# Kernel optimization log

Hardware: AMD Instinct MI355X
Metric: run time of the kernel (lower is better)

## Reference

```python
import jax, jax.numpy as jnp
import numpy as np

N_NODES = 100000
BN_EPS = 1e-5


def _linear_params(key, fan_in, fan_out):
    k1, k2 = jax.random.split(key)
    lim = 1.0 / np.sqrt(fan_in)
    W = jax.random.uniform(k1, (fan_in, fan_out), jnp.float32, -lim, lim)
    b = jax.random.uniform(k2, (fan_out,), jnp.float32, -lim, lim)
    return W, b


def setup_inputs() -> dict:
    key = jax.random.key(0)
    ks = jax.random.split(key, 24)
    in_ch, hid, tdim, L = 17, 64, 32, 2
    E = 1600000
    inp = {}
    inp["x"] = jax.random.normal(ks[0], (N_NODES, in_ch), jnp.float32)
    inp["edge_index"] = jax.random.randint(ks[1], (2, E), 0, N_NODES, jnp.int64)
    inp["edge_dts"] = jax.random.uniform(ks[2], (E,), jnp.float32) * 100.0
    inp["batch_size"] = 10000
    # TimeEncode params (learned, TGAT init)
    inp["basis_freq"] = jnp.asarray(1.0 / 10 ** np.linspace(0, 9, tdim), jnp.float32)
    inp["phase"] = jnp.zeros((tdim,), jnp.float32)
    # TMP edge MLP: in = 2*in_ch + tdim
    mi = 2 * in_ch + tdim
    inp["tmp_W1"], inp["tmp_b1"] = _linear_params(ks[3], mi, mi // 2)
    inp["tmp_W2"], inp["tmp_b2"] = _linear_params(ks[4], mi // 2, in_ch)
    inp["proj_W"], inp["proj_b"] = _linear_params(ks[5], in_ch, hid)
    # SMP layers (stacked over L)
    si = 2 * hid
    W1s, b1s, W2s, b2s = [], [], [], []
    for l in range(L):
        W1, b1 = _linear_params(ks[6 + 2 * l], si, si // 2)
        W2, b2 = _linear_params(ks[7 + 2 * l], si // 2, hid)
        W1s.append(W1); b1s.append(b1); W2s.append(W2); b2s.append(b2)
    inp["smp_W1"] = jnp.stack(W1s); inp["smp_b1"] = jnp.stack(b1s)
    inp["smp_W2"] = jnp.stack(W2s); inp["smp_b2"] = jnp.stack(b2s)
    inp["bn_gamma"] = jnp.ones((L, hid), jnp.float32)
    inp["bn_beta"] = jnp.zeros((L, hid), jnp.float32)
    # classifier head
    inp["clf_W1"], inp["clf_b1"] = _linear_params(ks[12], hid, hid)
    inp["clf_g1"] = jnp.ones((hid,), jnp.float32); inp["clf_bb1"] = jnp.zeros((hid,), jnp.float32)
    inp["clf_W2"], inp["clf_b2"] = _linear_params(ks[13], hid, hid // 2)
    inp["clf_g2"] = jnp.ones((hid // 2,), jnp.float32); inp["clf_bb2"] = jnp.zeros((hid // 2,), jnp.float32)
    inp["clf_W3"], inp["clf_b3"] = _linear_params(ks[14], hid // 2, 1)
    return inp


def _segment_mean(vals, idx, n):
    s = jax.ops.segment_sum(vals, idx, num_segments=n)
    c = jax.ops.segment_sum(jnp.ones((idx.shape[0], 1), vals.dtype), idx, num_segments=n)
    return s / jnp.maximum(c, 1.0)


def _bn(x, g, b):
    m = x.mean(0)
    v = x.var(0)
    return (x - m) * jax.lax.rsqrt(v + BN_EPS) * g + b


def reference(x, edge_index, edge_dts, batch_size, basis_freq, phase,
              tmp_W1, tmp_b1, tmp_W2, tmp_b2, proj_W, proj_b,
              smp_W1, smp_b1, smp_W2, smp_b2, bn_gamma, bn_beta,
              clf_W1, clf_b1, clf_g1, clf_bb1,
              clf_W2, clf_b2, clf_g2, clf_bb2, clf_W3, clf_b3):
    src, dst = edge_index[0], edge_index[1]  # x_j = x[src], x_i = x[dst]
    n = x.shape[0]
    # TimeEncode: cos(t * freq + phase)  -> [E, time_dim]
    rel = jnp.cos(edge_dts[:, None] * basis_freq + phase)
    # --- TMP conv (applied once) ---
    x_i = x[dst]
    m_in = jnp.concatenate([x_i, x[src], rel], axis=-1)
    p = jnp.tanh(jax.nn.relu(m_in @ tmp_W1 + tmp_b1) @ tmp_W2 + tmp_b2)
    msg = (2.0 * p - 1.0) * x_i  # (p - q) * x_i with q = 1 - p
    h = x + _segment_mean(msg, dst, n)
    # --- project to hidden ---
    h = h @ proj_W + proj_b
    # --- L SMP layers with BatchNorm + ReLU (dropout = eval/identity) ---
    L = smp_W1.shape[0]
    for l in range(L):
        h_i = h[dst]
        m_in = jnp.concatenate([h_i, h[src]], axis=-1)
        p = jnp.tanh(jax.nn.relu(m_in @ smp_W1[l] + smp_b1[l]) @ smp_W2[l] + smp_b2[l])
        h = h + _segment_mean((2.0 * p - 1.0) * h_i, dst, n)
        h = jax.nn.relu(_bn(h, bn_gamma[l], bn_beta[l]))
    # --- classifier on seed nodes ---
    z = h[:batch_size]
    z = jax.nn.relu(_bn(z @ clf_W1 + clf_b1, clf_g1, clf_bb1))
    z = jax.nn.relu(_bn(z @ clf_W2 + clf_b2, clf_g2, clf_bb2))
    return z @ clf_W3 + clf_b3  # [batch_size, 1] logits
```

## Files before the change

### kernel.cpp

```cpp
#include <hip/hip_runtime.h>
#include <hip/hip_bf16.h>


typedef float  f32x4 __attribute__((ext_vector_type(4)));
typedef short  s16x8 __attribute__((ext_vector_type(8)));

__device__ __forceinline__ float tanh_factor(float u) {
  float e = __expf(2.0f * u);
  return fmaf(-4.0f, __builtin_amdgcn_rcpf(e + 1.0f), 1.0f);
}

__device__ __forceinline__ void atomic_add_f32(float* p, float v) {
  unsafeAtomicAdd(p, v);
}

__device__ __forceinline__ unsigned short f2bf(float f) {
  __hip_bfloat16 b = __float2bfloat16(f);
  return *(unsigned short*)&b;
}
__device__ __forceinline__ float bf2f(unsigned short u) {
  unsigned int v = ((unsigned int)u) << 16;
  return *(float*)&v;
}

__global__ __launch_bounds__(256) void k_hist(
    const int* __restrict__ ei, int* __restrict__ cntI, int E)
{
  int e = blockIdx.x * 256 + threadIdx.x;
  if (e < E) atomicAdd(&cntI[__builtin_nontemporal_load(ei + E + e)], 1);
}

__global__ __launch_bounds__(256) void k_scan_block(
    const int* __restrict__ cntI, int* __restrict__ cursor,
    int* __restrict__ bsum, int N)
{
  __shared__ int s[256];
  const int t = threadIdx.x;
  int i = blockIdx.x * 256 + t;
  int v = (i < N) ? cntI[i] : 0;
  s[t] = v;
  for (int off = 1; off < 256; off <<= 1) {
    __syncthreads();
    int x = (t >= off) ? s[t - off] : 0;
    __syncthreads();
    s[t] += x;
  }
  __syncthreads();
  if (i < N) cursor[i] = s[t] - v;
  if (t == 255) bsum[blockIdx.x] = s[255];
}

__global__ __launch_bounds__(512) void k_scan_bsum(int* __restrict__ bsum, int nb)
{
  __shared__ int s[512];
  const int t = threadIdx.x;
  int v = (t < nb) ? bsum[t] : 0;
  s[t] = v;
  for (int off = 1; off < 512; off <<= 1) {
    __syncthreads();
    int x = (t >= off) ? s[t - off] : 0;
    __syncthreads();
    s[t] += x;
  }
  __syncthreads();
  if (t < nb) bsum[t] = s[t] - v;
}

__global__ __launch_bounds__(256) void k_expand_add(
    int* __restrict__ cursor, const int* __restrict__ bsum,
    const int* __restrict__ cntI, int* __restrict__ dstS, int N)
{
  int n = blockIdx.x * 256 + threadIdx.x;
  if (n >= N) return;
  int cur = cursor[n] + bsum[blockIdx.x];
  cursor[n] = cur;
  int c = cntI[n];
  for (int i = 0; i < c; i++) dstS[cur + i] = n;
}

__global__ __launch_bounds__(256) void k_scatter_x(
    const int* __restrict__ ei, const float* __restrict__ dts,
    int* __restrict__ cursor, int2* __restrict__ srcdtS, int E, int N)
{
  const int g  = blockIdx.x & 7;
  const int bi = blockIdx.x >> 3;
  const int nb = gridDim.x >> 3;
  const int lo = (int)(((long long)N * g) >> 3);
  const int hi = (int)(((long long)N * (g + 1)) >> 3);
  for (int e = bi * 256 + threadIdx.x; e < E; e += nb * 256) {
    int d = __builtin_nontemporal_load(ei + E + e);
    if (d >= lo && d < hi) {
      int s = __builtin_nontemporal_load(ei + e);
      float dt = __builtin_nontemporal_load(dts + e);
      int pos = atomicAdd(&cursor[d], 1);
      srcdtS[pos] = make_int2(s, __float_as_int(dt));
    }
  }
}

__global__ __launch_bounds__(256) void prep_all(
    const float* __restrict__ x, const float* __restrict__ tW1,
    const float* __restrict__ tW2, const float* __restrict__ sW1,
    const float* __restrict__ sW2, const float* __restrict__ cW1,
    const float* __restrict__ cW2, unsigned short* __restrict__ xb,
    unsigned short* __restrict__ W1t1, unsigned short* __restrict__ W2t1,
    unsigned short* __restrict__ W1t, unsigned short* __restrict__ W2t,
    unsigned short* __restrict__ cW1t, unsigned short* __restrict__ cW2t, int N)
{
  int i = blockIdx.x * 256 + threadIdx.x;
  int totalX = N * 24;
  for (int idx = i; idx < totalX; idx += gridDim.x * 256) {
    int n = idx / 24, c = idx - n * 24;
    xb[idx] = (c < 17) ? f2bf(x[n * 17 + c]) : (unsigned short)0;
  }
  if (i < 48 * 96) {
    int n = i / 96, k = i - n * 96;
    int src = (k < 17) ? k : (k >= 24 && k < 41) ? (k - 24 + 17)
            : (k >= 48 && k < 80) ? (k - 48 + 34) : -1;
    W1t1[i] = (n < 33 && src >= 0) ? f2bf(tW1[src * 33 + n]) : (unsigned short)0;
  }
  if (i < 32 * 64) {
    int n = i / 64, k = i - n * 64;
    W2t1[i] = (n < 17 && k < 33) ? f2bf(tW2[k * 17 + n]) : (unsigned short)0;
  }
  if (i < 2 * 64 * 128) {
    int l = i >> 13; int r = i & 8191; int n = r >> 7; int k = r & 127;
    W1t[i] = f2bf(sW1[((size_t)l * 128 + k) * 64 + n]);
  }
  if (i < 2 * 64 * 64) {
    int l = i >> 12; int r = i & 4095; int n = r >> 6; int k = r & 63;
    W2t[i] = f2bf(sW2[((size_t)l * 64 + k) * 64 + n]);
  }
  if (i < 64 * 64) {
    int c = i >> 6, k = i & 63;
    cW1t[i] = f2bf(cW1[k * 64 + c]);
  }
  if (i < 32 * 64) {
    int c = i >> 6, k = i & 63;
    cW2t[i] = f2bf(cW2[k * 32 + c]);
  }
}

__global__ __launch_bounds__(256, 3) void phase1_edge_mfma(
    const unsigned short* __restrict__ xb, const int* __restrict__ dstS,
    const int2* __restrict__ srcdtS, const float* __restrict__ freq,
    const float* __restrict__ phs,
    const unsigned short* __restrict__ W1t1, const float* __restrict__ b1,
    const unsigned short* __restrict__ W2t1, const float* __restrict__ b2,
    float* __restrict__ accum, int E, int nwt)
{
  __shared__ unsigned short sA[64][104];
  __shared__ unsigned short sHid[64][72];
  __shared__ float sRed[64][20];
  __shared__ int   sDst[64];

  const int t = threadIdx.x;
  const int wv = t >> 6, lane = t & 63, l16 = lane & 15, quad = lane >> 4;
  const int r0 = wv * 16;

  s16x8 w1f[3][3], w2f[2][2];
  float bias1[3], bias2[2];
#pragma unroll
  for (int cb = 0; cb < 3; cb++) {
    int n = cb * 16 + l16;
#pragma unroll
    for (int kb = 0; kb < 3; kb++)
      w1f[cb][kb] = *(const s16x8*)&W1t1[n * 96 + kb * 32 + quad * 8];
    bias1[cb] = (n < 33) ? b1[n] : 0.0f;
  }
#pragma unroll
  for (int cb = 0; cb < 2; cb++) {
    int n = cb * 16 + l16;
#pragma unroll
    for (int kb = 0; kb < 2; kb++)
      w2f[cb][kb] = *(const s16x8*)&W2t1[n * 64 + kb * 32 + quad * 8];
    bias2[cb] = (n < 17) ? b2[n] : 0.0f;
  }

  for (int i = lane; i < 16 * 28; i += 64) {
    int rr = r0 + i / 28, c = i % 28;
    int col = (c < 6) ? 18 + c : (c < 12) ? 42 + (c - 6) : 80 + (c - 12);
    sA[rr][col] = 0;
  }
  for (int i = lane; i < 256; i += 64)
    sHid[r0 + (i >> 4)][48 + (i & 15)] = 0;

  const int gw = blockIdx.x * 4 + wv;
  const int nw = gridDim.x * 4;

  for (int tile = gw; tile < nwt; tile += nw) {
    const int eb = tile << 4;

    {
      int e_loc = lane >> 2, q = lane & 3;
      int rr = r0 + e_loc;
      int er = eb + e_loc; if (er >= E) er = E - 1;
      if (q < 2) {
        int node = q ? srcdtS[er].x : dstS[er];
        if (!q) sDst[rr] = node;
        const unsigned short* src = &xb[(size_t)node * 24];
        int base = q ? 24 : 0;
        *(uint4*)&sA[rr][base]     = *(const uint4*)&src[0];
        *(uint4*)&sA[rr][base + 8] = *(const uint4*)&src[8];
        *(unsigned int*)&sA[rr][base + 16] = *(const unsigned int*)&src[16];
      } else {
        float dt = __int_as_float(srcdtS[er].y);
        int k0 = (q == 2) ? 0 : 16;
        unsigned short tmp[16] __attribute__((aligned(16)));
#pragma unroll
        for (int j = 0; j < 16; j++)
          tmp[j] = f2bf(__cosf(fmaf(dt, freq[k0 + j], phs[k0 + j])));
        *(uint4*)&sA[rr][48 + k0]     = *(const uint4*)&tmp[0];
        *(uint4*)&sA[rr][48 + k0 + 8] = *(const uint4*)&tmp[8];
      }
    }

    f32x4 a1[3];
#pragma unroll
    for (int cb = 0; cb < 3; cb++)
      a1[cb] = (f32x4){bias1[cb], bias1[cb], bias1[cb], bias1[cb]};
#pragma unroll
    for (int kb = 0; kb < 3; kb++) {
      s16x8 aF = *(const s16x8*)&sA[r0 + l16][kb * 32 + quad * 8];
#pragma unroll
      for (int cb = 0; cb < 3; cb++)
        a1[cb] = __builtin_amdgcn_mfma_f32_16x16x32_bf16(aF, w1f[cb][kb], a1[cb], 0, 0, 0);
    }
#pragma unroll
    for (int cb = 0; cb < 3; cb++)
#pragma unroll
      for (int reg = 0; reg < 4; reg++)
        sHid[r0 + quad * 4 + reg][cb * 16 + l16] = f2bf(fmaxf(a1[cb][reg], 0.0f));

    f32x4 a2[2];
#pragma unroll
    for (int cb = 0; cb < 2; cb++)
      a2[cb] = (f32x4){bias2[cb], bias2[cb], bias2[cb], bias2[cb]};
#pragma unroll
    for (int kb = 0; kb < 2; kb++) {
      s16x8 aF = *(const s16x8*)&sHid[r0 + l16][kb * 32 + quad * 8];
#pragma unroll
      for (int cb = 0; cb < 2; cb++)
        a2[cb] = __builtin_amdgcn_mfma_f32_16x16x32_bf16(aF, w2f[cb][kb], a2[cb], 0, 0, 0);
    }

#pragma unroll
    for (int reg = 0; reg < 4; reg++) {
      int row = r0 + quad * 4 + reg;
      bool ok = (eb + quad * 4 + reg < E);
      sRed[row][l16] = ok ? tanh_factor(a2[0][reg]) : 0.0f;
      if (l16 == 0) sRed[row][16] = ok ? tanh_factor(a2[1][reg]) : 0.0f;
    }

    if (lane < 17) {
      int col = lane;
      float run = 0.0f;
      int cur = sDst[r0];
#pragma unroll
      for (int k = 0; k < 16; k++) {
        int d = sDst[r0 + k];
        float v = sRed[r0 + k][col];
        if (d != cur) {
          atomic_add_f32(&accum[(size_t)cur * 17 + col], run);
          run = 0.0f; cur = d;
        }
        run += v;
      }
      atomic_add_f32(&accum[(size_t)cur * 17 + col], run);
    }
  }
}

__global__ __launch_bounds__(256) void phase1_node(
    const float* __restrict__ x, const float* __restrict__ acc1,
    const int* __restrict__ cntI, const float* __restrict__ Wp,
    const float* __restrict__ bp, float* __restrict__ h,
    float* __restrict__ acc2, int N)
{
  __shared__ float s0[4][20];
  const int t = threadIdx.x;
  const int nb = blockIdx.x << 2;
  if (t < 68) {
    int nl = t / 17, c = t % 17;
    int n = nb + nl;
    float v = 0.0f;
    if (n < N) {
      float cnt = fmaxf((float)cntI[n], 1.0f);
      v = x[n * 17 + c] * (1.0f + acc1[n * 17 + c] / cnt);
    }
    s0[nl][c] = v;
  }
  __syncthreads();
  int nl = t >> 6, j = t & 63;
  int n = nb + nl;
  if (n < N) {
    float acc = bp[j];
#pragma unroll
    for (int c = 0; c < 17; c++) acc = fmaf(s0[nl][c], Wp[c * 64 + j], acc);
    h[n * 64 + j] = acc;
    acc2[n * 64 + j] = 0.0f;
  }
}

template <bool DO_BN>
__global__ void prep_P(
    float* __restrict__ h, const unsigned short* __restrict__ W1t,
    const float* __restrict__ b1,
    const float* __restrict__ bns, const float* __restrict__ bnq,
    const float* __restrict__ gam, const float* __restrict__ bet, float invR,
    unsigned short* __restrict__ P1, unsigned short* __restrict__ P2, int N)
{
  __shared__ unsigned short sH[64][72];
  __shared__ float sM[64], sS[64], sB[64];
  const int t = threadIdx.x;
  const int wv = t >> 6, lane = t & 63, l16 = lane & 15, quad = lane >> 4;
  const int nb = blockIdx.x << 6;

  if (DO_BN) {
    if (t < 64) {
      float m = bns[t] * invR;
      float var = bnq[t] * invR - m * m;
      sM[t] = m;
      sS[t] = gam[t] * rsqrtf(var + 1e-5f);
      sB[t] = bet[t];
    }
    __syncthreads();
  }

#pragma unroll
  for (int i = 0; i < 4; i++) {
    int g = t + i * 256;
    int r = g >> 4, c4 = (g & 15) << 2;
    int n0 = nb + r;
    bool valid = (n0 < N);
    int n = valid ? n0 : N - 1;
    float4 v = *(const float4*)&h[(size_t)n * 64 + c4];
    if (DO_BN) {
      v.x = fmaxf(fmaf(v.x - sM[c4 + 0], sS[c4 + 0], sB[c4 + 0]), 0.0f);
      v.y = fmaxf(fmaf(v.y - sM[c4 + 1], sS[c4 + 1], sB[c4 + 1]), 0.0f);
      v.z = fmaxf(fmaf(v.z - sM[c4 + 2], sS[c4 + 2], sB[c4 + 2]), 0.0f);
      v.w = fmaxf(fmaf(v.w - sM[c4 + 3], sS[c4 + 3], sB[c4 + 3]), 0.0f);
      if (valid) *(float4*)&h[(size_t)n0 * 64 + c4] = v;
    }
    ushort4 o = { f2bf(v.x), f2bf(v.y), f2bf(v.z), f2bf(v.w) };
    *(ushort4*)&sH[r][c4] = o;
  }
  __syncthreads();

  const int n = nb + wv * 16 + l16;
#pragma unroll
  for (int half = 0; half < 2; half++) {
    f32x4 acc[4];
#pragma unroll
    for (int cb = 0; cb < 4; cb++) {
      if (half == 0) {
        float4 bv = *(const float4*)&b1[cb * 16 + quad * 4];
        acc[cb] = (f32x4){bv.x, bv.y, bv.z, bv.w};
      } else {
        acc[cb] = (f32x4){0.0f, 0.0f, 0.0f, 0.0f};
      }
    }
#pragma unroll
    for (int kb = 0; kb < 2; kb++) {
      s16x8 bF = *(const s16x8*)&sH[wv * 16 + l16][kb * 32 + quad * 8];
#pragma unroll
      for (int cb = 0; cb < 4; cb++) {
        s16x8 aF = *(const s16x8*)&W1t[(cb * 16 + l16) * 128 + half * 64 + kb * 32 + quad * 8];
        acc[cb] = __builtin_amdgcn_mfma_f32_16x16x32_bf16(aF, bF, acc[cb], 0, 0, 0);
      }
    }
    if (n < N) {
      unsigned short* P = half ? P2 : P1;
#pragma unroll
      for (int cb = 0; cb < 4; cb++) {
        ushort4 o = { f2bf(acc[cb][0]), f2bf(acc[cb][1]),
                      f2bf(acc[cb][2]), f2bf(acc[cb][3]) };
        *(ushort4*)&P[(size_t)n * 64 + cb * 16 + quad * 4] = o;
      }
    }
  }
}

__global__ __launch_bounds__(256, 4) void phase2_edge(
    const unsigned short* __restrict__ P1, const unsigned short* __restrict__ P2,
    const int* __restrict__ dstS, const int2* __restrict__ srcdtS,
    const unsigned short* __restrict__ W2t, const float* __restrict__ b2,
    float* __restrict__ accum, int E, int nwt)
{
  __shared__ unsigned short sA[64][136];
  __shared__ int sDst[64];
  float* sRedF = (float*)&sA[0][0];

  const int t = threadIdx.x;
  const int wv = t >> 6, lane = t & 63, l16 = lane & 15, quad = lane >> 4;
  const int r0 = wv * 16;

  s16x8 w2f[4][2];
  f32x4 bias2v[4];
#pragma unroll
  for (int cb = 0; cb < 4; cb++) {
#pragma unroll
    for (int kb = 0; kb < 2; kb++)
      w2f[cb][kb] = *(const s16x8*)&W2t[(cb * 16 + l16) * 64 + kb * 32 + quad * 8];
    float4 bv = *(const float4*)&b2[cb * 16 + quad * 4];
    bias2v[cb] = (f32x4){bv.x, bv.y, bv.z, bv.w};
  }

  const int gw = blockIdx.x * 4 + wv;
  const int nw = gridDim.x * 4;
  const int eRow = r0 + l16;

  for (int tile = gw; tile < nwt; tile += nw) {
    const int eb = tile << 4;

    {
      int e_loc = lane >> 2, q = lane & 3;
      int rr = r0 + e_loc;
      int er = eb + e_loc; if (er >= E) er = E - 1;
      int node;
      if (q < 2) { node = dstS[er]; if (!q) sDst[rr] = node; }
      else       node = srcdtS[er].x;
      const unsigned short* src = (q < 2 ? P1 : P2) + (size_t)node * 64 + (q & 1) * 32;
      int cb0 = q * 32;
#pragma unroll
      for (int j = 0; j < 4; j++)
        *(uint4*)&sA[rr][cb0 + j * 8] = *(const uint4*)&src[j * 8];
    }

    s16x8 hidf[2];
#pragma unroll
    for (int kb = 0; kb < 2; kb++) {
      s16x8 x1 = *(const s16x8*)&sA[eRow][kb * 32 + quad * 8];
      s16x8 x2 = *(const s16x8*)&sA[eRow][64 + kb * 32 + quad * 8];
      s16x8 hf;
#pragma unroll
      for (int j = 0; j < 8; j++) {
        float a = bf2f((unsigned short)x1[j]);
        float b = bf2f((unsigned short)x2[j]);
        hf[j] = (short)f2bf(fmaxf(a + b, 0.0f));
      }
      hidf[kb] = hf;
    }

    f32x4 acc[4];
#pragma unroll
    for (int cb = 0; cb < 4; cb++) acc[cb] = bias2v[cb];
#pragma unroll
    for (int kb = 0; kb < 2; kb++)
#pragma unroll
      for (int cb = 0; cb < 4; cb++)
        acc[cb] = __builtin_amdgcn_mfma_f32_16x16x32_bf16(w2f[cb][kb], hidf[kb], acc[cb], 0, 0, 0);

    bool ok = (eb + l16 < E);
#pragma unroll
    for (int cb = 0; cb < 4; cb++) {
      f32x4 f;
#pragma unroll
      for (int reg = 0; reg < 4; reg++)
        f[reg] = ok ? tanh_factor(acc[cb][reg]) : 0.0f;
      *(f32x4*)&sRedF[eRow * 68 + cb * 16 + quad * 4] = f;
    }

    {
      float run = 0.0f;
      int cur = sDst[r0];
#pragma unroll
      for (int k = 0; k < 16; k++) {
        int d = sDst[r0 + k];
        float v = sRedF[(r0 + k) * 68 + lane];
        if (d != cur) {
          atomic_add_f32(&accum[(size_t)cur * 64 + lane], run);
          run = 0.0f; cur = d;
        }
        run += v;
      }
      atomic_add_f32(&accum[(size_t)cur * 64 + lane], run);
    }
  }
}

__global__ __launch_bounds__(256) void node_update_bn(
    float* __restrict__ h, float* __restrict__ accum,
    const int* __restrict__ cntI, float* __restrict__ bns,
    float* __restrict__ bnq, int N)
{
  const int t = threadIdx.x;
  float ls = 0.0f, lq = 0.0f;
  int total = N * 64;
  for (int idx = blockIdx.x * 256 + t; idx < total; idx += gridDim.x * 256) {
    int n = idx >> 6;
    float cnt = fmaxf((float)cntI[n], 1.0f);
    float v = h[idx] * (1.0f + accum[idx] / cnt);
    accum[idx] = 0.0f;
    h[idx] = v;
    ls += v; lq += v * v;
  }
  __shared__ float ss[256], sq[256];
  ss[t] = ls; sq[t] = lq;
  __syncthreads();
  if (t < 64) {
    float s = ss[t] + ss[t + 64] + ss[t + 128] + ss[t + 192];
    float q = sq[t] + sq[t + 64] + sq[t + 128] + sq[t + 192];
    atomic_add_f32(&bns[t], s);
    atomic_add_f32(&bnq[t], q);
  }
}

template <int NCB>
__global__ __launch_bounds__(256) void clf_mfma(
    const float* __restrict__ in, const unsigned short* __restrict__ Wt,
    const float* __restrict__ bias, float* __restrict__ z,
    float* __restrict__ bns, float* __restrict__ bnq,
    const float* __restrict__ ibns, const float* __restrict__ ibnq,
    const float* __restrict__ igam, const float* __restrict__ ibet,
    float iinvR, int rows)
{
  __shared__ unsigned short sIn[64][72];
  __shared__ float sM[64], sS[64], sB[64];
  const int t = threadIdx.x;
  const int wv = t >> 6, lane = t & 63, l16 = lane & 15, quad = lane >> 4;
  const int nb = blockIdx.x << 6;

  if (t < 64) {
    float m = ibns[t] * iinvR;
    float var = ibnq[t] * iinvR - m * m;
    sM[t] = m;
    sS[t] = igam[t] * rsqrtf(var + 1e-5f);
    sB[t] = ibet[t];
  }

  s16x8 wf[NCB][2];
  f32x4 bv[NCB];
#pragma unroll
  for (int cb = 0; cb < NCB; cb++) {
#pragma unroll
    for (int kb = 0; kb < 2; kb++)
      wf[cb][kb] = *(const s16x8*)&Wt[(cb * 16 + l16) * 64 + kb * 32 + quad * 8];
    float4 b4 = *(const float4*)&bias[cb * 16 + quad * 4];
    bv[cb] = (f32x4){b4.x, b4.y, b4.z, b4.w};
  }
  __syncthreads();

#pragma unroll
  for (int i = 0; i < 4; i++) {
    int g = t + i * 256;
    int r = g >> 4, c4 = (g & 15) << 2;
    int n = nb + r; if (n >= rows) n = rows - 1;
    float4 v = *(const float4*)&in[(size_t)n * 64 + c4];
    v.x = fmaxf(fmaf(v.x - sM[c4 + 0], sS[c4 + 0], sB[c4 + 0]), 0.0f);
    v.y = fmaxf(fmaf(v.y - sM[c4 + 1], sS[c4 + 1], sB[c4 + 1]), 0.0f);
    v.z = fmaxf(fmaf(v.z - sM[c4 + 2], sS[c4 + 2], sB[c4 + 2]), 0.0f);
    v.w = fmaxf(fmaf(v.w - sM[c4 + 3], sS[c4 + 3], sB[c4 + 3]), 0.0f);
    ushort4 o = { f2bf(v.x), f2bf(v.y), f2bf(v.z), f2bf(v.w) };
    *(ushort4*)&sIn[r][c4] = o;
  }
  __syncthreads();

  const int n = nb + wv * 16 + l16;
  const bool ok = (n < rows);
  f32x4 acc[NCB];
#pragma unroll
  for (int cb = 0; cb < NCB; cb++) acc[cb] = bv[cb];
#pragma unroll
  for (int kb = 0; kb < 2; kb++) {
    s16x8 bF = *(const s16x8*)&sIn[wv * 16 + l16][kb * 32 + quad * 8];
#pragma unroll
    for (int cb = 0; cb < NCB; cb++)
      acc[cb] = __builtin_amdgcn_mfma_f32_16x16x32_bf16(wf[cb][kb], bF, acc[cb], 0, 0, 0);
  }

#pragma unroll
  for (int cb = 0; cb < NCB; cb++) {
    if (ok)
      *(float4*)&z[(size_t)n * (NCB * 16) + cb * 16 + quad * 4] =
          make_float4(acc[cb][0], acc[cb][1], acc[cb][2], acc[cb][3]);
    f32x4 s, q;
#pragma unroll
    for (int reg = 0; reg < 4; reg++) {
      float v = ok ? acc[cb][reg] : 0.0f;
      s[reg] = v; q[reg] = v * v;
    }
#pragma unroll
    for (int m = 1; m < 16; m <<= 1) {
#pragma unroll
      for (int reg = 0; reg < 4; reg++) {
        s[reg] += __shfl_xor(s[reg], m);
        q[reg] += __shfl_xor(q[reg], m);
      }
    }
    if (l16 == 0) {
#pragma unroll
      for (int reg = 0; reg < 4; reg++) {
        int col = cb * 16 + quad * 4 + reg;
        atomic_add_f32(&bns[col], s[reg]);
        atomic_add_f32(&bnq[col], q[reg]);
      }
    }
  }
}

__global__ __launch_bounds__(256) void clf_final(
    const float* __restrict__ z2, const float* __restrict__ W3,
    const float* __restrict__ b3,
    const float* __restrict__ ibns, const float* __restrict__ ibnq,
    const float* __restrict__ igam, const float* __restrict__ ibet,
    float iinvR, float* __restrict__ out, int rows)
{
  __shared__ float sM[32], sS[32], sB[32];
  const int t = threadIdx.x;
  if (t < 32) {
    float m = ibns[t] * iinvR;
    float var = ibnq[t] * iinvR - m * m;
    sM[t] = m;
    sS[t] = igam[t] * rsqrtf(var + 1e-5f);
    sB[t] = ibet[t];
  }
  __syncthreads();
  int n = blockIdx.x * 256 + t;
  if (n >= rows) return;
  float acc = b3[0];
#pragma unroll
  for (int k = 0; k < 32; k++) {
    float v = fmaxf(fmaf(z2[n * 32 + k] - sM[k], sS[k], sB[k]), 0.0f);
    acc = fmaf(v, W3[k], acc);
  }
  out[n] = acc;
}

extern "C" void kernel_launch(void* const* d_in, const int* in_sizes, int n_in,
                              void* d_out, int out_size, void* d_ws, size_t ws_size,
                              hipStream_t stream)
{
  const float* x    = (const float*)d_in[0];
  const int*   ei   = (const int*)  d_in[1];
  const float* dts  = (const float*)d_in[2];
  const float* freq = (const float*)d_in[4];
  const float* phs  = (const float*)d_in[5];
  const float* tW1  = (const float*)d_in[6];
  const float* tb1  = (const float*)d_in[7];
  const float* tW2  = (const float*)d_in[8];
  const float* tb2  = (const float*)d_in[9];
  const float* pW   = (const float*)d_in[10];
  const float* pb   = (const float*)d_in[11];
  const float* sW1  = (const float*)d_in[12];
  const float* sb1  = (const float*)d_in[13];
  const float* sW2  = (const float*)d_in[14];
  const float* sb2  = (const float*)d_in[15];
  const float* bng  = (const float*)d_in[16];
  const float* bnb  = (const float*)d_in[17];
  const float* cW1  = (const float*)d_in[18];
  const float* cb1  = (const float*)d_in[19];
  const float* cg1  = (const float*)d_in[20];
  const float* cbb1 = (const float*)d_in[21];
  const float* cW2  = (const float*)d_in[22];
  const float* cb2  = (const float*)d_in[23];
  const float* cg2  = (const float*)d_in[24];
  const float* cbb2 = (const float*)d_in[25];
  const float* cW3  = (const float*)d_in[26];
  const float* cb3  = (const float*)d_in[27];
  float* out = (float*)d_out;

  const int N = in_sizes[0] / 17;
  const int E = in_sizes[1] / 2;
  const int B = out_size;

  char* base = (char*)d_ws;
  size_t off = 0;
  float* h    = (float*)(base + off); off += (size_t)N * 64 * 4;
  float* acc2 = (float*)(base + off); off += (size_t)N * 64 * 4;
  char*  uni  = base + off;           off += (size_t)N * 64 * 4;
  float* bnsAll = (float*)(base + off); off += 8 * 64 * 4;
  unsigned short* W1t = (unsigned short*)(base + off); off += 2 * 64 * 128 * 2;
  unsigned short* W2t = (unsigned short*)(base + off); off += 2 * 64 * 64 * 2;
  unsigned short* cW1t = (unsigned short*)(base + off); off += 64 * 64 * 2;
  unsigned short* cW2t = (unsigned short*)(base + off); off += 32 * 64 * 2;
  int* cntI   = (int*)(base + off); off += (size_t)N * 4;
  int* cursor = (int*)(base + off); off += (size_t)N * 4;
  int* bsum   = (int*)(base + off); off += 512 * 4;
  int* dstS   = (int*)(base + off); off += (size_t)E * 4;
  off = (off + 15) & ~(size_t)15;
  int2* srcdtS = (int2*)(base + off); off += (size_t)E * 8;
  size_t needed = off;
  if (ws_size < needed) return;

  float* acc1 = (float*)uni;
  unsigned short* xb   = (unsigned short*)(uni + (size_t)N * 17 * 4);
  unsigned short* W1t1 = xb + (size_t)N * 24;
  unsigned short* W2t1 = W1t1 + 48 * 96;
  unsigned short* P1 = (unsigned short*)uni;
  unsigned short* P2 = P1 + (size_t)N * 64;
  float* z1 = (float*)uni;
  float* z2 = z1 + (size_t)B * 64;

  const int nwt = (E + 15) / 16;
  const int NB = (N + 255) / 256;
  if (NB > 512) return;

  hipMemsetAsync(cntI, 0, (size_t)N * 4, stream);
  hipMemsetAsync(acc1, 0, (size_t)N * 17 * 4, stream);
  hipMemsetAsync(bnsAll, 0, 8 * 64 * 4, stream);

  k_hist<<<(E + 255) / 256, 256, 0, stream>>>(ei, cntI, E);
  k_scan_block<<<NB, 256, 0, stream>>>(cntI, cursor, bsum, N);
  k_scan_bsum<<<1, 512, 0, stream>>>(bsum, NB);
  k_expand_add<<<NB, 256, 0, stream>>>(cursor, bsum, cntI, dstS, N);
  k_scatter_x<<<1024, 256, 0, stream>>>(ei, dts, cursor, srcdtS, E, N);
  prep_all<<<(N * 24 + 255) / 256, 256, 0, stream>>>(
      x, tW1, tW2, sW1, sW2, cW1, cW2, xb, W1t1, W2t1, W1t, W2t, cW1t, cW2t, N);

  phase1_edge_mfma<<<768, 256, 0, stream>>>(
      xb, dstS, srcdtS, freq, phs, W1t1, tb1, W2t1, tb2, acc1, E, nwt);
  phase1_node<<<(N + 3) / 4, 256, 0, stream>>>(x, acc1, cntI, pW, pb, h, acc2, N);

  const int PB = (N + 63) / 64;
  prep_P<false><<<PB, 256, 0, stream>>>(
      h, W1t, sb1, nullptr, nullptr, nullptr, nullptr, 0.0f, P1, P2, N);
  phase2_edge<<<1024, 256, 0, stream>>>(
      P1, P2, dstS, srcdtS, W2t, sb2, acc2, E, nwt);
  node_update_bn<<<1024, 256, 0, stream>>>(h, acc2, cntI,
                                           bnsAll + 0, bnsAll + 64, N);
  prep_P<true><<<PB, 256, 0, stream>>>(
      h, W1t + (size_t)64 * 128, sb1 + 64, bnsAll + 0, bnsAll + 64,
      bng, bnb, 1.0f / (float)N, P1, P2, N);
  phase2_edge<<<1024, 256, 0, stream>>>(
      P1, P2, dstS, srcdtS, W2t + (size_t)64 * 64, sb2 + 64, acc2, E, nwt);
  node_update_bn<<<1024, 256, 0, stream>>>(h, acc2, cntI,
                                           bnsAll + 128, bnsAll + 192, N);

  const int CB = (B + 63) / 64;
  clf_mfma<4><<<CB, 256, 0, stream>>>(
      h, cW1t, cb1, z1, bnsAll + 256, bnsAll + 320,
      bnsAll + 128, bnsAll + 192, bng + 64, bnb + 64, 1.0f / (float)N, B);
  clf_mfma<2><<<CB, 256, 0, stream>>>(
      z1, cW2t, cb2, z2, bnsAll + 384, bnsAll + 448,
      bnsAll + 256, bnsAll + 320, cg1, cbb1, 1.0f / (float)B, B);
  clf_final<<<(B + 255) / 256, 256, 0, stream>>>(
      z2, cW3, cb3, bnsAll + 384, bnsAll + 448, cg2, cbb2,
      1.0f / (float)B, out, B);
}
```

Measured before the change: 862.2 us.

## Prefetch next tile's gathered rows into registers and make segment dst uniform

In the TMP and SMP edge kernels, the gather of node rows and edge indices for the next tile is issued into registers before the current tile's MFMA work. This lets the random-access global loads overlap with compute instead of stalling at the start of each tile. Destination indices used in the segmented reduction are also read with readfirstlane so the compiler treats them as wave-uniform scalars. The cost is higher register pressure, and one extra redundant gather on the final iteration.

```diff
diff --git a/kernel.cpp b/kernel.cpp
--- a/kernel.cpp
+++ b/kernel.cpp
@@ -188,32 +188,44 @@
   const int gw = blockIdx.x * 4 + wv;
   const int nw = gridDim.x * 4;
 
+  const int e_loc = lane >> 2, q = lane & 3;
+  const int rr = r0 + e_loc;
+
+  int ndP = 0; uint4 xa0, xa1; unsigned int xa2 = 0; float dtP = 0.0f;
+  auto issue = [&](int tt) {
+    int er = (tt << 4) + e_loc; if (er >= E) er = E - 1;
+    if (q < 2) {
+      ndP = q ? srcdtS[er].x : dstS[er];
+      const unsigned short* src = &xb[(size_t)ndP * 24];
+      xa0 = *(const uint4*)&src[0];
+      xa1 = *(const uint4*)&src[8];
+      xa2 = *(const unsigned int*)&src[16];
+    } else {
+      dtP = __int_as_float(srcdtS[er].y);
+    }
+  };
+  issue(gw < nwt ? gw : 0);
+
   for (int tile = gw; tile < nwt; tile += nw) {
     const int eb = tile << 4;
 
-    {
-      int e_loc = lane >> 2, q = lane & 3;
-      int rr = r0 + e_loc;
-      int er = eb + e_loc; if (er >= E) er = E - 1;
-      if (q < 2) {
-        int node = q ? srcdtS[er].x : dstS[er];
-        if (!q) sDst[rr] = node;
-        const unsigned short* src = &xb[(size_t)node * 24];
-        int base = q ? 24 : 0;
-        *(uint4*)&sA[rr][base]     = *(const uint4*)&src[0];
-        *(uint4*)&sA[rr][base + 8] = *(const uint4*)&src[8];
-        *(unsigned int*)&sA[rr][base + 16] = *(const unsigned int*)&src[16];
-      } else {
-        float dt = __int_as_float(srcdtS[er].y);
-        int k0 = (q == 2) ? 0 : 16;
-        unsigned short tmp[16] __attribute__((aligned(16)));
-#pragma unroll
-        for (int j = 0; j < 16; j++)
-          tmp[j] = f2bf(__cosf(fmaf(dt, freq[k0 + j], phs[k0 + j])));
-        *(uint4*)&sA[rr][48 + k0]     = *(const uint4*)&tmp[0];
-        *(uint4*)&sA[rr][48 + k0 + 8] = *(const uint4*)&tmp[8];
-      }
-    }
+    if (q < 2) {
+      if (!q) sDst[rr] = ndP;
+      const int base = q ? 24 : 0;
+      *(uint4*)&sA[rr][base]     = xa0;
+      *(uint4*)&sA[rr][base + 8] = xa1;
+      *(unsigned int*)&sA[rr][base + 16] = xa2;
+    } else {
+      const int k0 = (q == 2) ? 0 : 16;
+      unsigned short tmp[16] __attribute__((aligned(16)));
+#pragma unroll
+      for (int j = 0; j < 16; j++)
+        tmp[j] = f2bf(__cosf(fmaf(dtP, freq[k0 + j], phs[k0 + j])));
+      *(uint4*)&sA[rr][48 + k0]     = *(const uint4*)&tmp[0];
+      *(uint4*)&sA[rr][48 + k0 + 8] = *(const uint4*)&tmp[8];
+    }
+
+    { int nt = tile + nw; issue(nt < nwt ? nt : tile); }
 
     f32x4 a1[3];
 #pragma unroll
@@ -255,10 +267,10 @@
     if (lane < 17) {
       int col = lane;
       float run = 0.0f;
-      int cur = sDst[r0];
+      int cur = __builtin_amdgcn_readfirstlane(sDst[r0]);
 #pragma unroll
       for (int k = 0; k < 16; k++) {
-        int d = sDst[r0 + k];
+        int d = __builtin_amdgcn_readfirstlane(sDst[r0 + k]);
         float v = sRed[r0 + k][col];
         if (d != cur) {
           atomic_add_f32(&accum[(size_t)cur * 17 + col], run);
@@ -410,22 +422,34 @@
   const int nw = gridDim.x * 4;
   const int eRow = r0 + l16;
 
+  const int e_loc = lane >> 2, q = lane & 3;
+  const int rr = r0 + e_loc;
+  const unsigned short* const Pb = (q < 2) ? P1 : P2;
+  const int cb0 = q * 32;
+  const size_t sub = (size_t)((q & 1) * 32);
+
+  int ndP = 0; uint4 pA, pB, pC, pD;
+  auto issue = [&](int tt) {
+    int er = (tt << 4) + e_loc; if (er >= E) er = E - 1;
+    ndP = (q < 2) ? dstS[er] : srcdtS[er].x;
+    const unsigned short* src = Pb + (size_t)ndP * 64 + sub;
+    pA = *(const uint4*)&src[0];
+    pB = *(const uint4*)&src[8];
+    pC = *(const uint4*)&src[16];
+    pD = *(const uint4*)&src[24];
+  };
+  issue(gw < nwt ? gw : 0);
+
   for (int tile = gw; tile < nwt; tile += nw) {
     const int eb = tile << 4;
 
-    {
-      int e_loc = lane >> 2, q = lane & 3;
-      int rr = r0 + e_loc;
-      int er = eb + e_loc; if (er >= E) er = E - 1;
-      int node;
-      if (q < 2) { node = dstS[er]; if (!q) sDst[rr] = node; }
-      else       node = srcdtS[er].x;
-      const unsigned short* src = (q < 2 ? P1 : P2) + (size_t)node * 64 + (q & 1) * 32;
-      int cb0 = q * 32;
-#pragma unroll
-      for (int j = 0; j < 4; j++)
-        *(uint4*)&sA[rr][cb0 + j * 8] = *(const uint4*)&src[j * 8];
-    }
+    if (q == 0) sDst[rr] = ndP;
+    *(uint4*)&sA[rr][cb0]      = pA;
+    *(uint4*)&sA[rr][cb0 + 8]  = pB;
+    *(uint4*)&sA[rr][cb0 + 16] = pC;
+    *(uint4*)&sA[rr][cb0 + 24] = pD;
+
+    { int nt = tile + nw; issue(nt < nwt ? nt : tile); }
 
     s16x8 hidf[2];
 #pragma unroll
@@ -463,10 +487,10 @@
 
     {
       float run = 0.0f;
-      int cur = sDst[r0];
+      int cur = __builtin_amdgcn_readfirstlane(sDst[r0]);
 #pragma unroll
       for (int k = 0; k < 16; k++) {
-        int d = sDst[r0 + k];
+        int d = __builtin_amdgcn_readfirstlane(sDst[r0 + k]);
         float v = sRedF[(r0 + k) * 68 + lane];
         if (d != cur) {
           atomic_add_f32(&accum[(size_t)cur * 64 + lane], run);
```

After: 826.1 us. -4.2%, faster.
